# Performance work log

Hardware: AMD Instinct MI355X
Metric: run time of the kernel (lower is better)

## Reference

```python
import jax, jax.numpy as jnp
import numpy as np

N_CH, LONG, LAT = 8, 64, 64
N = N_CH * LONG * LAT          # 32768 flattened node count
OUT = 16 * 16                  # output_size ** 2
BATCH = 512


def _build_adjacency(n, long_, lat):
    # Faithful reconstruction of the (intended) COO pattern in GNNLayer.__init__.
    rows, cols, vals = [], [], []
    for k in range(n):
        for j in range(0, long_ * lat, 3):
            rows += [k + j, k + j, j]
            cols += [k + j, j, k + j]
            vals += [1.0, 1.0, 1.0]
        for i in range(lat + 1, (long_ - 1) * lat - 1, 3):
            offs = [i - 1, i + 1, i + lat, i - lat,
                    i + lat - 1, i + lat + 1, i - lat - 1, i - lat + 1]
            for o in offs:
                rows.append(i); cols.append(k + o); vals.append(1.0)
            for o in offs:
                rows.append(k + o); cols.append(i); vals.append(1.0)
    return (np.asarray(rows, np.int32), np.asarray(cols, np.int32),
            np.asarray(vals, np.float32))


def setup_inputs() -> dict:
    key = jax.random.key(0)
    k1, k2, k3 = jax.random.split(key, 3)
    rows, cols, vals = _build_adjacency(N_CH, LONG, LAT)
    x = jax.random.normal(k1, (BATCH, N_CH, LONG, LAT), jnp.float32)
    W = jax.random.normal(k2, (OUT, N), jnp.float32) / np.sqrt(N)  # lin1.weight
    b = jax.random.normal(k3, (OUT,), jnp.float32) * 0.01          # lin1.bias
    return {"x": x, "W": W, "b": b,
            "vals": jnp.asarray(vals),
            "rows": jnp.asarray(rows), "cols": jnp.asarray(cols)}


def reference(x, W, b, vals, rows, cols):
    B = x.shape[0]
    xf = x.reshape(B, -1)                    # [B, N]
    # SpMM with duplicate-index accumulation (matches torch COO coalescing):
    gathered = xf[:, cols] * vals            # [B, nnz]
    h1 = jax.ops.segment_sum(gathered.T, rows, num_segments=N).T  # [B, N]
    return h1 @ W.T + b                      # [B, 256]
```

## Files before the change

### kernel.cpp

```cpp
#include <hip/hip_runtime.h>
#include <hip/hip_bf16.h>

#define N_NODES 32768
#define OUT_F   256
#define BATCH   512
#define ROWS_CAP 4352
#define KS       17
#define KSLICE   256
#define TB_RB    (ROWS_CAP / 32)
#define TB_BLOCKS (TB_RB * (OUT_F / 32))
#define OUT_BLOCKS ((BATCH * OUT_F) / 256)
#define GBM 64
#define GBN 64


typedef __attribute__((ext_vector_type(8))) short short8;
typedef __attribute__((ext_vector_type(4))) float f32x4;

__device__ __forceinline__ float bf2f(ushort u) {
    return __uint_as_float(((unsigned)u) << 16);
}
__device__ __forceinline__ ushort f2bf(float f) {
    unsigned u = __float_as_uint(f);
    return (ushort)((u + 0x7fffu + ((u >> 16) & 1u)) >> 16);
}
__device__ __forceinline__ bool inJ(int x) { return x >= 0 && x <= 4095 && x % 3 == 0; }
__device__ __forceinline__ bool inI(int x) { return x >= 65 && x <= 4028 && x % 3 == 2; }

__global__ __launch_bounds__(256) void k_prep(const float* __restrict__ W,
                                              ushort* __restrict__ Wtb,
                                              const float* __restrict__ bias,
                                              float* __restrict__ out) {
    int bid = blockIdx.x, t = threadIdx.x;
    if (bid < TB_BLOCKS) {
        __shared__ float tile[32][33];
        int rb = (bid % TB_RB) * 32;
        int ob = (bid / TB_RB) * 32;
        int tx = t & 31, ty = t >> 5;
        #pragma unroll
        for (int s = 0; s < 32; s += 8)
            tile[ty + s][tx] = W[(long)(ob + ty + s) * N_NODES + rb + tx];
        __syncthreads();
        #pragma unroll
        for (int s = 0; s < 32; s += 8)
            Wtb[(long)(rb + ty + s) * OUT_F + ob + tx] = f2bf(tile[tx][ty + s]);
        return;
    }
    int idx = (bid - TB_BLOCKS) * 256 + t;
    out[idx] = bias[idx & (OUT_F - 1)];
}

__global__ __launch_bounds__(256) void k_fold(const ushort* __restrict__ Wtb,
                                              ushort* __restrict__ wbfT) {
    const int soff[30] = {-65,-64,-63,-62,-61,-60,-59,-58,-57,-56,
                           -1,  0,  1,  2,  3,  4,  5,  6,  7,  8,
                           63, 64, 65, 66, 67, 68, 69, 70, 71, 72};
    const float smul[30] = {1,2,3,3,3,3,3,3,2,1,
                            1,1,2,2,2,2,2,2,1,1,
                            1,2,3,3,3,3,3,3,2,1};
    int c = blockIdx.x * 4 + (threadIdx.x >> 6);
    int lane4 = (threadIdx.x & 63) * 4;
    float ax = 0, ay = 0, az = 0, aw = 0;
    #define ADDW(r, m) { \
        ushort4 w_ = *(const ushort4*)(Wtb + (long)(r) * OUT_F + lane4); \
        ax += (m) * bf2f(w_.x); ay += (m) * bf2f(w_.y); \
        az += (m) * bf2f(w_.z); aw += (m) * bf2f(w_.w); }
    int m1 = 0;
    #pragma unroll
    for (int k = 0; k < 8; ++k) {
        int j = c - k;
        if (inJ(j)) { ++m1; ADDW(j, 1.0f); }
    }
    if (m1) ADDW(c, (float)m1);
    if (inJ(c)) {
        #pragma unroll
        for (int k = 0; k < 8; ++k) ADDW(c + k, 1.0f);
    }
    #pragma unroll
    for (int q = 0; q < 30; ++q) {
        int i = c - soff[q];
        if (inI(i)) ADDW(i, smul[q]);
    }
    if (inI(c)) {
        #pragma unroll
        for (int q = 0; q < 30; ++q) ADDW(c + soff[q], smul[q]);
    }
    #undef ADDW
    ushort4 o;
    o.x = f2bf(ax); o.y = f2bf(ay); o.z = f2bf(az); o.w = f2bf(aw);
    *(ushort4*)(wbfT + (long)c * OUT_F + lane4) = o;
}

__global__ __launch_bounds__(256) void k_gemm(const float* __restrict__ xf,
                                              const ushort* __restrict__ wbfT,
                                              float* __restrict__ out) {
    __shared__ ushort Ash[GBM * 40];
    __shared__ ushort Bsh[GBN * 40];
    int t = threadIdx.x;
    int w = t >> 6, lane = t & 63;
    int lrow = lane & 15, lseg = lane >> 4;
    int gm0 = blockIdx.x * GBM, gn0 = blockIdx.y * GBN, k0 = blockIdx.z * KSLICE;
    f32x4 acc[4] = {};
    for (int ks = 0; ks < KSLICE; ks += 32) {
        int kb = k0 + ks;
        __syncthreads();
        {
            int row = t >> 2, kc = (t & 3) * 8;
            float4 x0 = *(const float4*)(xf + (long)(gm0 + row) * N_NODES + kb + kc);
            float4 x1 = *(const float4*)(xf + (long)(gm0 + row) * N_NODES + kb + kc + 4);
            short8 v;
            v[0] = (short)f2bf(x0.x); v[1] = (short)f2bf(x0.y);
            v[2] = (short)f2bf(x0.z); v[3] = (short)f2bf(x0.w);
            v[4] = (short)f2bf(x1.x); v[5] = (short)f2bf(x1.y);
            v[6] = (short)f2bf(x1.z); v[7] = (short)f2bf(x1.w);
            *(short8*)(Ash + row * 40 + kc) = v;
        }
        {
            int k = t >> 3, n8 = (t & 7) * 8;
            short8 v = *(const short8*)(wbfT + (long)(kb + k) * OUT_F + gn0 + n8);
            int gk = k >> 3, klo = k & 7;
            #pragma unroll
            for (int j = 0; j < 8; ++j) {
                int n = n8 + j;
                Bsh[n * 40 + ((gk ^ ((n >> 3) & 3)) << 3) + klo] = (ushort)v[j];
            }
        }
        __syncthreads();
        short8 af = *(const short8*)(Ash + (w * 16 + lrow) * 40 + lseg * 8);
        #pragma unroll
        for (int f = 0; f < 4; ++f) {
            int n = f * 16 + lrow;
            short8 bf = *(const short8*)(Bsh + n * 40 + ((lseg ^ ((n >> 3) & 3)) << 3));
            acc[f] = __builtin_amdgcn_mfma_f32_16x16x32_bf16(af, bf, acc[f], 0, 0, 0);
        }
    }
    #pragma unroll
    for (int f = 0; f < 4; ++f)
        #pragma unroll
        for (int i = 0; i < 4; ++i) {
            int rowg = gm0 + w * 16 + lseg * 4 + i;
            int colg = gn0 + f * 16 + lrow;
            atomicAdd(&out[(long)rowg * OUT_F + colg], acc[f][i]);
        }
}

extern "C" void kernel_launch(void* const* d_in, const int* in_sizes, int n_in,
                              void* d_out, int out_size, void* d_ws, size_t ws_size,
                              hipStream_t stream) {
    const float* xf   = (const float*)d_in[0];
    const float* W    = (const float*)d_in[1];
    const float* bias = (const float*)d_in[2];

    char* base = (char*)d_ws;
    ushort* Wtb  = (ushort*)base;
    ushort* wbfT = Wtb + (size_t)ROWS_CAP * OUT_F;

    k_prep<<<TB_BLOCKS + OUT_BLOCKS, 256, 0, stream>>>(W, Wtb, bias, (float*)d_out);

    k_fold<<<ROWS_CAP / 4, 256, 0, stream>>>(Wtb, wbfT);

    k_gemm<<<dim3(BATCH / GBM, OUT_F / GBN, KS), 256, 0, stream>>>(xf, wbfT, (float*)d_out);
}
```

Before: 33.37 us.

## Fuse weight transpose and stencil fold via LDS halo tiles; pre-convert x to bf16

Merges the weight transpose and the adjacency fold into one kernel. Each block stages a haloed window of W rows, converted to bf16, into LDS and computes the folded weights from there, which removes the intermediate transposed-weight buffer and one kernel launch. The same launch also converts the used slice of x to bf16 once, so the GEMM loads bf16 directly instead of converting fp32 on every tile. In exchange, each fold tile rereads a 72-row halo of W (redundant global reads), the bf16 x buffer adds an extra write and read, and the large LDS tile may limit occupancy.

```diff
diff --git a/kernel.cpp b/kernel.cpp
--- a/kernel.cpp
+++ b/kernel.cpp
@@ -7,11 +7,14 @@
 #define ROWS_CAP 4352
 #define KS       17
 #define KSLICE   256
-#define TB_RB    (ROWS_CAP / 32)
-#define TB_BLOCKS (TB_RB * (OUT_F / 32))
-#define OUT_BLOCKS ((BATCH * OUT_F) / 256)
 #define GBM 64
 #define GBN 64
+#define FOLD_BLOCKS ((ROWS_CAP / 16) * 2)
+#define CV_BLOCKS   ((BATCH * ROWS_CAP / 8) / 256)
+#define OUT_BLOCKS  ((BATCH * OUT_F) / 256)
+#define WIN   160
+#define HALO  72
+#define PITCH 132
 
 
 typedef __attribute__((ext_vector_type(8))) short short8;
@@ -27,71 +30,95 @@
 __device__ __forceinline__ bool inJ(int x) { return x >= 0 && x <= 4095 && x % 3 == 0; }
 __device__ __forceinline__ bool inI(int x) { return x >= 65 && x <= 4028 && x % 3 == 2; }
 
-__global__ __launch_bounds__(256) void k_prep(const float* __restrict__ W,
-                                              ushort* __restrict__ Wtb,
-                                              const float* __restrict__ bias,
-                                              float* __restrict__ out) {
+__global__ __launch_bounds__(256) void k_fused(const float* __restrict__ W,
+                                               const float* __restrict__ xf,
+                                               const float* __restrict__ bias,
+                                               ushort* __restrict__ wbfT,
+                                               ushort* __restrict__ xbf,
+                                               float* __restrict__ out) {
+    __shared__ ushort lt[WIN * PITCH];
     int bid = blockIdx.x, t = threadIdx.x;
-    if (bid < TB_BLOCKS) {
-        __shared__ float tile[32][33];
-        int rb = (bid % TB_RB) * 32;
-        int ob = (bid / TB_RB) * 32;
-        int tx = t & 31, ty = t >> 5;
+    if (bid < FOLD_BLOCKS) {
+        int tile = bid >> 1, oh = bid & 1;
+        int c0 = tile * 16, o0 = oh * 128;
+        int rbase = c0 - HALO;
+        {
+            int o_local = t & 127, rh = t >> 7;
+            const float* wrow = W + (long)(o0 + o_local) * N_NODES;
+            #pragma unroll
+            for (int rr = 0; rr < 80; rr += 4) {
+                int ri = rh * 80 + rr;
+                int r = rbase + ri;
+                float4 v = (r >= 0) ? *(const float4*)(wrow + r)
+                                    : make_float4(0.f, 0.f, 0.f, 0.f);
+                lt[(ri + 0) * PITCH + o_local] = f2bf(v.x);
+                lt[(ri + 1) * PITCH + o_local] = f2bf(v.y);
+                lt[(ri + 2) * PITCH + o_local] = f2bf(v.z);
+                lt[(ri + 3) * PITCH + o_local] = f2bf(v.w);
+            }
+        }
+        __syncthreads();
+        const int soff[30] = {-65,-64,-63,-62,-61,-60,-59,-58,-57,-56,
+                               -1,  0,  1,  2,  3,  4,  5,  6,  7,  8,
+                               63, 64, 65, 66, 67, 68, 69, 70, 71, 72};
+        const float smul[30] = {1,2,3,3,3,3,3,3,2,1,
+                                1,1,2,2,2,2,2,2,1,1,
+                                1,2,3,3,3,3,3,3,2,1};
+        int w = t >> 6, lane = t & 63;
+        int ol2 = lane * 2;
         #pragma unroll
-        for (int s = 0; s < 32; s += 8)
-            tile[ty + s][tx] = W[(long)(ob + ty + s) * N_NODES + rb + tx];
-        __syncthreads();
-        #pragma unroll
-        for (int s = 0; s < 32; s += 8)
-            Wtb[(long)(rb + ty + s) * OUT_F + ob + tx] = f2bf(tile[tx][ty + s]);
+        for (int p = 0; p < 4; ++p) {
+            int c = c0 + w * 4 + p;
+            float ax = 0, ay = 0;
+            #define ADDW(r, m) { \
+                ushort2 w_ = *(const ushort2*)&lt[((r) - rbase) * PITCH + ol2]; \
+                ax += (m) * bf2f(w_.x); ay += (m) * bf2f(w_.y); }
+            int m1 = 0;
+            #pragma unroll
+            for (int k = 0; k < 8; ++k) {
+                int j = c - k;
+                if (inJ(j)) { ++m1; ADDW(j, 1.0f); }
+            }
+            if (m1) ADDW(c, (float)m1);
+            if (inJ(c)) {
+                #pragma unroll
+                for (int k = 0; k < 8; ++k) ADDW(c + k, 1.0f);
+            }
+            #pragma unroll
+            for (int q = 0; q < 30; ++q) {
+                int i = c - soff[q];
+                if (inI(i)) ADDW(i, smul[q]);
+            }
+            if (inI(c)) {
+                #pragma unroll
+                for (int q = 0; q < 30; ++q) ADDW(c + soff[q], smul[q]);
+            }
+            #undef ADDW
+            ushort2 o2;
+            o2.x = f2bf(ax); o2.y = f2bf(ay);
+            *(ushort2*)(wbfT + (long)c * OUT_F + o0 + ol2) = o2;
+        }
         return;
     }
-    int idx = (bid - TB_BLOCKS) * 256 + t;
+    if (bid < FOLD_BLOCKS + CV_BLOCKS) {
+        int idx = (bid - FOLD_BLOCKS) * 256 + t;
+        int b  = idx / (ROWS_CAP / 8);
+        int kc = (idx % (ROWS_CAP / 8)) * 8;
+        float4 x0 = *(const float4*)(xf + (long)b * N_NODES + kc);
+        float4 x1 = *(const float4*)(xf + (long)b * N_NODES + kc + 4);
+        short8 o;
+        o[0] = (short)f2bf(x0.x); o[1] = (short)f2bf(x0.y);
+        o[2] = (short)f2bf(x0.z); o[3] = (short)f2bf(x0.w);
+        o[4] = (short)f2bf(x1.x); o[5] = (short)f2bf(x1.y);
+        o[6] = (short)f2bf(x1.z); o[7] = (short)f2bf(x1.w);
+        *(short8*)(xbf + (long)b * ROWS_CAP + kc) = o;
+        return;
+    }
+    int idx = (bid - FOLD_BLOCKS - CV_BLOCKS) * 256 + t;
     out[idx] = bias[idx & (OUT_F - 1)];
 }
 
-__global__ __launch_bounds__(256) void k_fold(const ushort* __restrict__ Wtb,
-                                              ushort* __restrict__ wbfT) {
-    const int soff[30] = {-65,-64,-63,-62,-61,-60,-59,-58,-57,-56,
-                           -1,  0,  1,  2,  3,  4,  5,  6,  7,  8,
-                           63, 64, 65, 66, 67, 68, 69, 70, 71, 72};
-    const float smul[30] = {1,2,3,3,3,3,3,3,2,1,
-                            1,1,2,2,2,2,2,2,1,1,
-                            1,2,3,3,3,3,3,3,2,1};
-    int c = blockIdx.x * 4 + (threadIdx.x >> 6);
-    int lane4 = (threadIdx.x & 63) * 4;
-    float ax = 0, ay = 0, az = 0, aw = 0;
-    #define ADDW(r, m) { \
-        ushort4 w_ = *(const ushort4*)(Wtb + (long)(r) * OUT_F + lane4); \
-        ax += (m) * bf2f(w_.x); ay += (m) * bf2f(w_.y); \
-        az += (m) * bf2f(w_.z); aw += (m) * bf2f(w_.w); }
-    int m1 = 0;
-    #pragma unroll
-    for (int k = 0; k < 8; ++k) {
-        int j = c - k;
-        if (inJ(j)) { ++m1; ADDW(j, 1.0f); }
-    }
-    if (m1) ADDW(c, (float)m1);
-    if (inJ(c)) {
-        #pragma unroll
-        for (int k = 0; k < 8; ++k) ADDW(c + k, 1.0f);
-    }
-    #pragma unroll
-    for (int q = 0; q < 30; ++q) {
-        int i = c - soff[q];
-        if (inI(i)) ADDW(i, smul[q]);
-    }
-    if (inI(c)) {
-        #pragma unroll
-        for (int q = 0; q < 30; ++q) ADDW(c + soff[q], smul[q]);
-    }
-    #undef ADDW
-    ushort4 o;
-    o.x = f2bf(ax); o.y = f2bf(ay); o.z = f2bf(az); o.w = f2bf(aw);
-    *(ushort4*)(wbfT + (long)c * OUT_F + lane4) = o;
-}
-
-__global__ __launch_bounds__(256) void k_gemm(const float* __restrict__ xf,
+__global__ __launch_bounds__(256) void k_gemm(const ushort* __restrict__ xbf,
                                               const ushort* __restrict__ wbfT,
                                               float* __restrict__ out) {
     __shared__ ushort Ash[GBM * 40];
@@ -106,13 +133,7 @@
         __syncthreads();
         {
             int row = t >> 2, kc = (t & 3) * 8;
-            float4 x0 = *(const float4*)(xf + (long)(gm0 + row) * N_NODES + kb + kc);
-            float4 x1 = *(const float4*)(xf + (long)(gm0 + row) * N_NODES + kb + kc + 4);
-            short8 v;
-            v[0] = (short)f2bf(x0.x); v[1] = (short)f2bf(x0.y);
-            v[2] = (short)f2bf(x0.z); v[3] = (short)f2bf(x0.w);
-            v[4] = (short)f2bf(x1.x); v[5] = (short)f2bf(x1.y);
-            v[6] = (short)f2bf(x1.z); v[7] = (short)f2bf(x1.w);
+            short8 v = *(const short8*)(xbf + (long)(gm0 + row) * ROWS_CAP + kb + kc);
             *(short8*)(Ash + row * 40 + kc) = v;
         }
         {
@@ -152,12 +173,11 @@
     const float* bias = (const float*)d_in[2];
 
     char* base = (char*)d_ws;
-    ushort* Wtb  = (ushort*)base;
-    ushort* wbfT = Wtb + (size_t)ROWS_CAP * OUT_F;
+    ushort* wbfT = (ushort*)base;
+    ushort* xbf  = wbfT + (size_t)ROWS_CAP * OUT_F;
 
-    k_prep<<<TB_BLOCKS + OUT_BLOCKS, 256, 0, stream>>>(W, Wtb, bias, (float*)d_out);
+    k_fused<<<FOLD_BLOCKS + CV_BLOCKS + OUT_BLOCKS, 256, 0, stream>>>(
+        W, xf, bias, wbfT, xbf, (float*)d_out);
 
-    k_fold<<<ROWS_CAP / 4, 256, 0, stream>>>(Wtb, wbfT);
-
-    k_gemm<<<dim3(BATCH / GBM, OUT_F / GBN, KS), 256, 0, stream>>>(xf, wbfT, (float*)d_out);
+    k_gemm<<<dim3(BATCH / GBM, OUT_F / GBN, KS), 256, 0, stream>>>(xbf, wbfT, (float*)d_out);
 }
```

Result: slower. 40.50 us (+21.4%).
